# Kernel optimization log

Hardware: AMD Instinct MI355X
Metric: run time of the kernel (lower is better)

## Reference

```python
import jax, jax.numpy as jnp
import numpy as np

B, NH, NPTS = 16, 64, 2048
NEIGHS = 20   # knn neighbors in EdgeConv
K_SEL = 512   # topk points selected
EPS = 1e-5    # BatchNorm eps


def setup_inputs() -> dict:
    key = jax.random.key(0)
    ks = jax.random.split(key, 8)
    xyz = jax.random.normal(ks[0], (B, 3, NPTS), jnp.float32)
    seq1 = jax.random.normal(ks[1], (B, NH, NPTS), jnp.float32)
    perm = jax.random.permutation(ks[2], NPTS)
    # fc: Conv1d(n_h,n_h,1) + BN1d (eval-mode stats)
    W_fc = jax.random.normal(ks[3], (NH, NH), jnp.float32) * 0.1
    b_fc = jnp.zeros((NH,), jnp.float32)
    bn1_gamma = jnp.ones((NH,), jnp.float32)
    bn1_beta = jnp.zeros((NH,), jnp.float32)
    bn1_mean = jnp.zeros((NH,), jnp.float32)
    bn1_var = jnp.ones((NH,), jnp.float32)
    # EdgeConv: Conv2d(2*n_h, n_h, 1, bias=False) + BN2d
    W_ec = jax.random.normal(ks[4], (NH, 2 * NH), jnp.float32) * 0.05
    bn2_gamma = jnp.ones((NH,), jnp.float32)
    bn2_beta = jnp.zeros((NH,), jnp.float32)
    bn2_mean = jnp.zeros((NH,), jnp.float32)
    bn2_var = jnp.ones((NH,), jnp.float32)
    # Discriminator Bilinear(n_h, n_h, 1), xavier-uniform weight, zero bias
    lim = float(np.sqrt(6.0 / (NH + NH)))
    W_b = jax.random.uniform(ks[5], (NH, NH), jnp.float32, -lim, lim)
    b_b = jnp.zeros((), jnp.float32)
    return dict(xyz=xyz, seq1=seq1, perm=perm, W_fc=W_fc, b_fc=b_fc,
                bn1_gamma=bn1_gamma, bn1_beta=bn1_beta, bn1_mean=bn1_mean, bn1_var=bn1_var,
                W_ec=W_ec, bn2_gamma=bn2_gamma, bn2_beta=bn2_beta, bn2_mean=bn2_mean, bn2_var=bn2_var,
                W_b=W_b, b_b=b_b)


def reference(xyz, seq1, perm, W_fc, b_fc, bn1_gamma, bn1_beta, bn1_mean, bn1_var,
              W_ec, bn2_gamma, bn2_beta, bn2_mean, bn2_var, W_b, b_b):
    def fc(x):  # x: [B, NH, N] -> Conv1d(1x1) + BN1d(eval) + ReLU
        y = jnp.einsum('oc,bcn->bon', W_fc, x) + b_fc[None, :, None]
        scale = bn1_gamma / jnp.sqrt(bn1_var + EPS)
        y = (y - bn1_mean[None, :, None]) * scale[None, :, None] + bn1_beta[None, :, None]
        return jax.nn.relu(y)

    seq2 = seq1[:, :, perm]                       # shuffled negative sample
    h1 = fc(seq1)                                 # [B, NH, N]
    h2 = fc(seq2)

    # --- EdgeConv(center): knn in feature space ---
    x2 = jnp.sum(h1 * h1, axis=1)                 # [B, N]
    d = 2.0 * jnp.einsum('bcn,bcm->bnm', h1, h1) - x2[:, :, None] - x2[:, None, :]
    _, nidx = jax.lax.top_k(d, NEIGHS)            # [B, N, K] nearest neighbors

    pts = jnp.transpose(h1, (0, 2, 1))            # [B, N, NH]
    nb = jax.vmap(lambda p, i: p[i])(pts, nidx)   # [B, N, K, NH] gather
    ctr = jnp.broadcast_to(pts[:, :, None, :], nb.shape)
    feat = jnp.concatenate([nb - ctr, ctr], axis=-1)   # [B, N, K, 2*NH]

    y = jnp.einsum('bnkc,oc->bnko', feat, W_ec)   # 1x1 conv
    scale2 = bn2_gamma / jnp.sqrt(bn2_var + EPS)
    y = (y - bn2_mean) * scale2 + bn2_beta        # BN2d over channel (last axis)
    y = jnp.where(y >= 0, y, 0.2 * y)             # LeakyReLU(0.2)
    hn1 = jnp.max(y, axis=2)                      # max over k -> [B, N, NH]

    X = jax.nn.sigmoid(hn1)                       # summary per point, [B, N, NH]

    # --- Discriminator: Bilinear(n_h, n_h, 1) ---
    h1t = pts                                     # [B, N, NH]
    h2t = jnp.transpose(h2, (0, 2, 1))
    sc1 = jnp.einsum('bnc,cd,bnd->bn', h1t, W_b, X) + b_b
    sc2 = jnp.einsum('bnc,cd,bnd->bn', h2t, W_b, X) + b_b
    ret = jnp.concatenate([sc1, sc2], axis=1)     # [B, 2N]

    scores = jax.nn.sigmoid(sc1)                  # ret[:, :N]
    values, idx = jax.lax.top_k(scores, K_SEL)    # [B, K_SEL]

    gi = idx[:, None, :]
    seq_static = jnp.take_along_axis(seq1, jnp.broadcast_to(gi, (B, NH, K_SEL)), axis=2)
    seq = seq_static * values[:, None, :]
    xyz_static = jnp.take_along_axis(xyz, jnp.broadcast_to(gi, (B, 3, K_SEL)), axis=2)
    xyz_out = xyz_static * values[:, None, :]
    return seq, values, idx, ret, xyz_static, xyz_out
```

## Files before the change

kernel.cpp:

```cpp
#include <hip/hip_runtime.h>
#include <math.h>

#define NB 16
#define NH 64
#define NPTS 2048
#define NEIGHS 20
#define KSEL 512
#define EPSV 1e-5f

#define OFF_SEQ 0
#define OFF_VAL (NB*NH*KSEL)
#define OFF_IDX (OFF_VAL + NB*KSEL)
#define OFF_RET (OFF_IDX + NB*KSEL)
#define OFF_XST (OFF_RET + NB*2*NPTS)
#define OFF_XO  (OFF_XST + NB*3*KSEL)

__global__ __launch_bounds__(64) void k_fc(const float* __restrict__ seq1,
                                           const float* __restrict__ Wfc,
                                           const float* __restrict__ bfc,
                                           const float* __restrict__ b1g,
                                           const float* __restrict__ b1b,
                                           const float* __restrict__ b1m,
                                           const float* __restrict__ b1v,
                                           const float* __restrict__ Wec,
                                           float* __restrict__ pts,
                                           float* __restrict__ G1,
                                           float* __restrict__ G2,
                                           float* __restrict__ x2) {
  const int b = blockIdx.y, n0 = blockIdx.x * 64, l = threadIdx.x;
  const int n = n0 + l;
  __shared__ float ptL[64*65];
  const float* sq = seq1 + (size_t)b*NH*NPTS + n;
  float x[64];
  #pragma unroll
  for (int c = 0; c < 64; ++c) x[c] = sq[(size_t)c*NPTS];
  const size_t rowOff = ((size_t)b*NPTS + n)*NH;
  for (int o = 0; o < 64; ++o) {
    float acc = 0.f;
    const float* ar = Wfc + o*64;
    #pragma unroll
    for (int c = 0; c < 64; c += 4) {
      float4 a4 = *(const float4*)(ar + c);
      acc = fmaf(a4.x, x[c],   acc);
      acc = fmaf(a4.y, x[c+1], acc);
      acc = fmaf(a4.z, x[c+2], acc);
      acc = fmaf(a4.w, x[c+3], acc);
    }
    float s1 = b1g[o] / sqrtf(b1v[o] + EPSV);
    float y  = (acc + bfc[o] - b1m[o]) * s1 + b1b[o];
    y = fmaxf(y, 0.f);
    ptL[l*65 + o] = y;
    pts[rowOff + o] = y;
  }
  float pt[64];
  #pragma unroll
  for (int c = 0; c < 64; ++c) pt[c] = ptL[l*65 + c];
  float s2 = 0.f;
  #pragma unroll
  for (int c = 0; c < 64; ++c) s2 = fmaf(pt[c], pt[c], s2);
  x2[(size_t)b*NPTS + n] = s2;
  for (int o = 0; o < 64; ++o) {
    const float* w1 = Wec + o*128;
    float a1 = 0.f, a2 = 0.f;
    #pragma unroll
    for (int c = 0; c < 64; c += 4) {
      float4 u = *(const float4*)(w1 + c);
      float4 v = *(const float4*)(w1 + 64 + c);
      a1 = fmaf(u.x, pt[c],   a1); a1 = fmaf(u.y, pt[c+1], a1);
      a1 = fmaf(u.z, pt[c+2], a1); a1 = fmaf(u.w, pt[c+3], a1);
      a2 = fmaf(v.x, pt[c],   a2); a2 = fmaf(v.y, pt[c+1], a2);
      a2 = fmaf(v.z, pt[c+2], a2); a2 = fmaf(v.w, pt[c+3], a2);
    }
    G1[rowOff + o] = a1;
    G2[rowOff + o] = a2;
  }
}

#define DST 67
#define CSTR 68

__global__ __launch_bounds__(256) void k_knn(const float* __restrict__ pts,
                                             const float* __restrict__ x2,
                                             int* __restrict__ nidx) {
  const int b = blockIdx.y;
  const int row0 = blockIdx.x * 64;
  const int tid = threadIdx.x;
  const int rg = tid >> 4, cg = tid & 15;
  const int l = tid & 63, w = tid >> 6;

  __shared__ float smem[13056];
  float* rowS = smem;
  float* colS = smem + 4352;
  float* dS   = smem + 8704;
  float* x2S  = smem + 12992;

  const float* ptsb = pts + (size_t)b*NPTS*NH;

  {
    int rr = tid & 63, f0 = (tid >> 6) * 16;
    const float* src = ptsb + (size_t)(row0 + rr)*NH + f0;
    #pragma unroll
    for (int q = 0; q < 4; ++q)
      *(float4*)&rowS[rr*CSTR + f0 + 4*q] = *(const float4*)(src + 4*q);
  }

  float Lv[20]; int Li[20];
  #pragma unroll
  for (int k = 0; k < 20; ++k) { Lv[k] = -3.0e38f; Li[k] = 0x7fffffff; }

  for (int ct = 0; ct < NPTS; ct += 64) {
    __syncthreads();
    {
      int cl = tid & 63, f0 = (tid >> 6) * 16;
      const float* src = ptsb + (size_t)(ct + cl)*NH + f0;
      #pragma unroll
      for (int q = 0; q < 4; ++q)
        *(float4*)&colS[cl*CSTR + f0 + 4*q] = *(const float4*)(src + 4*q);
      if (tid < 64) x2S[tid] = x2[(size_t)b*NPTS + ct + tid];
    }
    __syncthreads();
    {
      float acc[4][4];
      #pragma unroll
      for (int i = 0; i < 4; ++i)
        #pragma unroll
        for (int j = 0; j < 4; ++j) acc[i][j] = 0.f;
      #pragma unroll
      for (int c = 0; c < NH; c += 4) {
        float4 rv[4], cv[4];
        #pragma unroll
        for (int i = 0; i < 4; ++i) rv[i] = *(const float4*)&rowS[(rg*4+i)*CSTR + c];
        #pragma unroll
        for (int j = 0; j < 4; ++j) cv[j] = *(const float4*)&colS[(cg+16*j)*CSTR + c];
        #pragma unroll
        for (int i = 0; i < 4; ++i)
          #pragma unroll
          for (int j = 0; j < 4; ++j) {
            acc[i][j] = fmaf(rv[i].x, cv[j].x, acc[i][j]);
            acc[i][j] = fmaf(rv[i].y, cv[j].y, acc[i][j]);
            acc[i][j] = fmaf(rv[i].z, cv[j].z, acc[i][j]);
            acc[i][j] = fmaf(rv[i].w, cv[j].w, acc[i][j]);
          }
      }
      #pragma unroll
      for (int i = 0; i < 4; ++i)
        #pragma unroll
        for (int j = 0; j < 4; ++j) {
          int cc = cg + 16*j;
          dS[(rg*4+i)*DST + cc] = fmaf(2.0f, acc[i][j], -x2S[cc]);
        }
    }
    __syncthreads();
    {
      #pragma unroll
      for (int s = 0; s < 16; ++s) {
        float v = dS[l*DST + w*16 + s];
        int  ci = ct + w*16 + s;
        if (v > Lv[19]) {
          float cv = v; int cidx = ci;
          #pragma unroll
          for (int k = 0; k < 20; ++k) {
            bool c = cv > Lv[k];
            float nv = c ? cv : Lv[k];
            int   ni = c ? cidx : Li[k];
            float ov = Lv[k]; int oi = Li[k];
            cv   = c ? ov : cv;
            cidx = c ? oi : cidx;
            Lv[k] = nv; Li[k] = ni;
          }
        }
      }
    }
  }

  __syncthreads();
  float* mV = smem;
  int*   mI = (int*)smem + 5120;
  #pragma unroll
  for (int k = 0; k < 20; ++k) {
    mV[(w*64 + l)*20 + k] = Lv[k];
    mI[(w*64 + l)*20 + k] = Li[k];
  }
  __syncthreads();
  if (w == 0) {
    for (int ws = 1; ws < 4; ++ws) {
      #pragma unroll
      for (int k = 0; k < 20; ++k) {
        float cv = mV[(ws*64 + l)*20 + k];
        int   ci = mI[(ws*64 + l)*20 + k];
        bool ins = (cv > Lv[19]) || (cv == Lv[19] && ci < Li[19]);
        if (ins) {
          float c0 = cv; int i0 = ci;
          #pragma unroll
          for (int k2 = 0; k2 < 20; ++k2) {
            bool c = (c0 > Lv[k2]) || (c0 == Lv[k2] && i0 < Li[k2]);
            float nv = c ? c0 : Lv[k2];
            int   ni = c ? i0 : Li[k2];
            float ov = Lv[k2]; int oi = Li[k2];
            c0 = c ? ov : c0;
            i0 = c ? oi : i0;
            Lv[k2] = nv; Li[k2] = ni;
          }
        }
      }
    }
    int* dst = nidx + ((size_t)b*NPTS + row0 + l)*NEIGHS;
    #pragma unroll
    for (int k = 0; k < 20; ++k) dst[k] = Li[k];
  }
}

__global__ __launch_bounds__(256) void k_score(const float* __restrict__ pts,
    const float* __restrict__ G1, const float* __restrict__ G2,
    const int* __restrict__ nidx, const int* __restrict__ perm,
    const float* __restrict__ Wb,
    const float* __restrict__ b2g, const float* __restrict__ b2b,
    const float* __restrict__ b2m, const float* __restrict__ b2v,
    const float* __restrict__ bb,
    float* __restrict__ sc1w, float* __restrict__ out) {
  const int b = blockIdx.y;
  const int n0 = blockIdx.x * 16;
  const int tid = threadIdx.x, l = tid & 63, w = tid >> 6;
  __shared__ float WbS[64*65];
  for (int i = tid; i < 64*64; i += 256) WbS[(i >> 6)*65 + (i & 63)] = Wb[i];
  __syncthreads();
  const float sc2v = b2g[l] / sqrtf(b2v[l] + EPSV);
  const float mean2 = b2m[l], beta2 = b2b[l];
  const float bbv = bb[0];
  const float* G1b = G1 + (size_t)b*NPTS*NH;
  for (int it = 0; it < 4; ++it) {
    const int n = n0 + it*4 + w;
    const size_t ro = (size_t)b*NPTS*NH + (size_t)n*NH;
    const float base = G2[ro + l] - G1[ro + l];
    const int* nb = nidx + ((size_t)b*NPTS + n)*NEIGHS;
    float mx = -3.0e38f;
    #pragma unroll
    for (int k = 0; k < NEIGHS; ++k) {
      int m = nb[k];
      float val = G1b[(size_t)m*NH + l] + base;
      float y = (val - mean2) * sc2v + beta2;
      y = (y >= 0.f) ? y : 0.2f*y;
      mx = fmaxf(mx, y);
    }
    float X = 1.f / (1.f + expf(-mx));
    double v = 0.0;
    #pragma unroll
    for (int d = 0; d < 64; ++d) {
      float xd = __shfl(X, d, 64);
      v += (double)WbS[l*65 + d] * (double)xd;
    }
    float p1 = pts[ro + l];
    int pn = perm[n];
    float p2 = pts[(size_t)b*NPTS*NH + (size_t)pn*NH + l];
    double s1 = (double)p1 * v;
    double s2 = (double)p2 * v;
    #pragma unroll
    for (int off = 32; off > 0; off >>= 1) {
      s1 += __shfl_xor(s1, off, 64);
      s2 += __shfl_xor(s2, off, 64);
    }
    if (l == 0) {
      float r1 = (float)(s1 + (double)bbv);
      float r2 = (float)(s2 + (double)bbv);
      sc1w[(size_t)b*NPTS + n] = r1;
      out[OFF_RET + (size_t)b*2*NPTS + n] = r1;
      out[OFF_RET + (size_t)b*2*NPTS + NPTS + n] = r2;
    }
  }
}

__global__ __launch_bounds__(256) void k_select(const float* __restrict__ sc1w,
    const float* __restrict__ seq1, const float* __restrict__ xyz,
    float* __restrict__ out) {
  const int b = blockIdx.x, tid = threadIdx.x;
  __shared__ unsigned long long keys[NPTS];
  __shared__ float valS[KSEL];
  __shared__ int idxS[KSEL];
  for (int i = tid; i < NPTS; i += 256) {
    float f = sc1w[(size_t)b*NPTS + i];
    unsigned u = __float_as_uint(f);
    u = (u & 0x80000000u) ? ~u : (u | 0x80000000u);
    keys[i] = ((unsigned long long)(~u) << 32) | (unsigned)i;
  }
  __syncthreads();
  for (int k = 2; k <= NPTS; k <<= 1) {
    for (int j = k >> 1; j > 0; j >>= 1) {
      for (int i = tid; i < NPTS; i += 256) {
        int l2 = i ^ j;
        if (l2 > i) {
          unsigned long long a = keys[i], c = keys[l2];
          bool up = ((i & k) == 0);
          if ((a > c) == up) { keys[i] = c; keys[l2] = a; }
        }
      }
      __syncthreads();
    }
  }
  for (int i = tid; i < KSEL; i += 256) {
    unsigned long long key = keys[i];
    int sidx = (int)(key & 0xffffffffULL);
    unsigned u = ~(unsigned)(key >> 32);
    unsigned fb = (u & 0x80000000u) ? (u & 0x7fffffffu) : ~u;
    float f = __uint_as_float(fb);
    float val = 1.f / (1.f + expf(-f));
    valS[i] = val; idxS[i] = sidx;
    out[OFF_VAL + (size_t)b*KSEL + i] = val;
    out[OFF_IDX + (size_t)b*KSEL + i] = (float)sidx;
  }
  __syncthreads();
  for (int t = tid; t < NH*KSEL; t += 256) {
    int c = t >> 9, i = t & (KSEL-1);
    float sv = seq1[((size_t)b*NH + c)*NPTS + idxS[i]];
    out[OFF_SEQ + (((size_t)b*NH + c) << 9) + i] = sv * valS[i];
  }
  for (int t = tid; t < 3*KSEL; t += 256) {
    int c = t >> 9, i = t & (KSEL-1);
    float xv = xyz[((size_t)b*3 + c)*NPTS + idxS[i]];
    out[OFF_XST + (((size_t)b*3 + c) << 9) + i] = xv;
    out[OFF_XO  + (((size_t)b*3 + c) << 9) + i] = xv * valS[i];
  }
}

extern "C" void kernel_launch(void* const* d_in, const int* in_sizes, int n_in,
                              void* d_out, int out_size, void* d_ws, size_t ws_size,
                              hipStream_t stream) {
  const float* xyz  = (const float*)d_in[0];
  const float* seq1 = (const float*)d_in[1];
  const int*   perm = (const int*)d_in[2];
  const float* Wfc  = (const float*)d_in[3];
  const float* bfc  = (const float*)d_in[4];
  const float* b1g  = (const float*)d_in[5];
  const float* b1b  = (const float*)d_in[6];
  const float* b1m  = (const float*)d_in[7];
  const float* b1v  = (const float*)d_in[8];
  const float* Wec  = (const float*)d_in[9];
  const float* b2g  = (const float*)d_in[10];
  const float* b2b  = (const float*)d_in[11];
  const float* b2m  = (const float*)d_in[12];
  const float* b2v  = (const float*)d_in[13];
  const float* Wb   = (const float*)d_in[14];
  const float* bb   = (const float*)d_in[15];
  float* out = (float*)d_out;

  float* ws   = (float*)d_ws;
  float* pts  = ws;
  float* G1   = pts + (size_t)NB*NPTS*NH;
  float* G2   = G1  + (size_t)NB*NPTS*NH;
  float* x2   = G2  + (size_t)NB*NPTS*NH;
  float* sc1w = x2  + (size_t)NB*NPTS;
  int*   nidx = (int*)(sc1w + (size_t)NB*NPTS);

  hipLaunchKernelGGL(k_fc, dim3(NPTS/64, NB), dim3(64), 0, stream,
                     seq1, Wfc, bfc, b1g, b1b, b1m, b1v, Wec, pts, G1, G2, x2);
  hipLaunchKernelGGL(k_knn, dim3(NPTS/64, NB), dim3(256), 0, stream,
                     pts, x2, nidx);
  hipLaunchKernelGGL(k_score, dim3(NPTS/16, NB), dim3(256), 0, stream,
                     pts, G1, G2, nidx, perm, Wb, b2g, b2b, b2m, b2v, bb, sc1w, out);
  hipLaunchKernelGGL(k_select, dim3(NB), dim3(256), 0, stream,
                     sc1w, seq1, xyz, out);
}
```

Before: 793.5 us.

## Buffer knn candidates per lane to cut divergent top-20 insertions; coalesce fc stores

In the knn kernel, candidates that beat the current 20th-best go into a small per-lane FIFO of four entries. The full top-20 insertion only runs when some lane in the wave has filled its buffer, so each wave takes the divergent insertion path less often. The fc kernel now stages pts, G1 and G2 through shared memory and writes them transposed so global stores are coalesced, at the cost of extra barriers and a split Wec loop. Buffered candidates are checked against a stale threshold, so more of them may be inserted, and the extra registers could lower occupancy.

```diff
diff --git a/kernel.cpp b/kernel.cpp
--- a/kernel.cpp
+++ b/kernel.cpp
@@ -7,6 +7,7 @@
 #define NEIGHS 20
 #define KSEL 512
 #define EPSV 1e-5f
+#define NINF -3.0e38f
 
 #define OFF_SEQ 0
 #define OFF_VAL (NB*NH*KSEL)
@@ -14,6 +15,23 @@
 #define OFF_RET (OFF_IDX + NB*KSEL)
 #define OFF_XST (OFF_RET + NB*2*NPTS)
 #define OFF_XO  (OFF_XST + NB*3*KSEL)
+
+__device__ __forceinline__ bool better(float av, int ai, float bv, int bi) {
+  return (av > bv) || (av == bv && ai < bi);
+}
+
+__device__ __forceinline__ void ins20(float (&Lv)[20], int (&Li)[20], float cv, int ci) {
+  #pragma unroll
+  for (int k = 0; k < 20; ++k) {
+    bool c = cv > Lv[k];
+    float nv = c ? cv : Lv[k];
+    int   ni = c ? ci : Li[k];
+    float ov = Lv[k]; int oi = Li[k];
+    cv = c ? ov : cv;
+    ci = c ? oi : ci;
+    Lv[k] = nv; Li[k] = ni;
+  }
+}
 
 __global__ __launch_bounds__(64) void k_fc(const float* __restrict__ seq1,
                                            const float* __restrict__ Wfc,
@@ -34,7 +52,7 @@
   float x[64];
   #pragma unroll
   for (int c = 0; c < 64; ++c) x[c] = sq[(size_t)c*NPTS];
-  const size_t rowOff = ((size_t)b*NPTS + n)*NH;
+
   for (int o = 0; o < 64; ++o) {
     float acc = 0.f;
     const float* ar = Wfc + o*64;
@@ -48,32 +66,53 @@
     }
     float s1 = b1g[o] / sqrtf(b1v[o] + EPSV);
     float y  = (acc + bfc[o] - b1m[o]) * s1 + b1b[o];
-    y = fmaxf(y, 0.f);
-    ptL[l*65 + o] = y;
-    pts[rowOff + o] = y;
+    ptL[l*65 + o] = fmaxf(y, 0.f);
   }
   float pt[64];
   #pragma unroll
   for (int c = 0; c < 64; ++c) pt[c] = ptL[l*65 + c];
-  float s2 = 0.f;
-  #pragma unroll
-  for (int c = 0; c < 64; ++c) s2 = fmaf(pt[c], pt[c], s2);
-  x2[(size_t)b*NPTS + n] = s2;
+  {
+    float s2 = 0.f;
+    #pragma unroll
+    for (int c = 0; c < 64; ++c) s2 = fmaf(pt[c], pt[c], s2);
+    x2[(size_t)b*NPTS + n] = s2;
+  }
+  const size_t base = ((size_t)b*NPTS + n0)*NH;
+  __syncthreads();
+  #pragma unroll 4
+  for (int t = 0; t < 64; ++t) pts[base + t*64 + l] = ptL[t*65 + l];
+  __syncthreads();
+
   for (int o = 0; o < 64; ++o) {
     const float* w1 = Wec + o*128;
-    float a1 = 0.f, a2 = 0.f;
+    float a1 = 0.f;
     #pragma unroll
     for (int c = 0; c < 64; c += 4) {
       float4 u = *(const float4*)(w1 + c);
-      float4 v = *(const float4*)(w1 + 64 + c);
       a1 = fmaf(u.x, pt[c],   a1); a1 = fmaf(u.y, pt[c+1], a1);
       a1 = fmaf(u.z, pt[c+2], a1); a1 = fmaf(u.w, pt[c+3], a1);
+    }
+    ptL[l*65 + o] = a1;
+  }
+  __syncthreads();
+  #pragma unroll 4
+  for (int t = 0; t < 64; ++t) G1[base + t*64 + l] = ptL[t*65 + l];
+  __syncthreads();
+
+  for (int o = 0; o < 64; ++o) {
+    const float* w2 = Wec + o*128 + 64;
+    float a2 = 0.f;
+    #pragma unroll
+    for (int c = 0; c < 64; c += 4) {
+      float4 v = *(const float4*)(w2 + c);
       a2 = fmaf(v.x, pt[c],   a2); a2 = fmaf(v.y, pt[c+1], a2);
       a2 = fmaf(v.z, pt[c+2], a2); a2 = fmaf(v.w, pt[c+3], a2);
     }
-    G1[rowOff + o] = a1;
-    G2[rowOff + o] = a2;
-  }
+    ptL[l*65 + o] = a2;
+  }
+  __syncthreads();
+  #pragma unroll 4
+  for (int t = 0; t < 64; ++t) G2[base + t*64 + l] = ptL[t*65 + l];
 }
 
 #define DST 67
@@ -106,16 +145,19 @@
 
   float Lv[20]; int Li[20];
   #pragma unroll
-  for (int k = 0; k < 20; ++k) { Lv[k] = -3.0e38f; Li[k] = 0x7fffffff; }
+  for (int k = 0; k < 20; ++k) { Lv[k] = NINF; Li[k] = 0x7fffffff; }
+  float f0v = NINF, f1v = NINF, f2v = NINF, f3v = NINF;
+  int   f0i = 0,    f1i = 0,    f2i = 0,    f3i = 0;
+  int   cnt = 0;
 
   for (int ct = 0; ct < NPTS; ct += 64) {
     __syncthreads();
     {
-      int cl = tid & 63, f0 = (tid >> 6) * 16;
-      const float* src = ptsb + (size_t)(ct + cl)*NH + f0;
+      int cl = tid & 63, f0_ = (tid >> 6) * 16;
+      const float* src = ptsb + (size_t)(ct + cl)*NH + f0_;
       #pragma unroll
       for (int q = 0; q < 4; ++q)
-        *(float4*)&colS[cl*CSTR + f0 + 4*q] = *(const float4*)(src + 4*q);
+        *(float4*)&colS[cl*CSTR + f0_ + 4*q] = *(const float4*)(src + 4*q);
       if (tid < 64) x2S[tid] = x2[(size_t)b*NPTS + ct + tid];
     }
     __syncthreads();
@@ -152,24 +194,36 @@
     }
     __syncthreads();
     {
+      const float* dRow = dS + l*DST + w*16;
       #pragma unroll
       for (int s = 0; s < 16; ++s) {
-        float v = dS[l*DST + w*16 + s];
+        float v = dRow[s];
         int  ci = ct + w*16 + s;
-        if (v > Lv[19]) {
-          float cv = v; int cidx = ci;
-          #pragma unroll
-          for (int k = 0; k < 20; ++k) {
-            bool c = cv > Lv[k];
-            float nv = c ? cv : Lv[k];
-            int   ni = c ? cidx : Li[k];
-            float ov = Lv[k]; int oi = Li[k];
-            cv   = c ? ov : cv;
-            cidx = c ? oi : cidx;
-            Lv[k] = nv; Li[k] = ni;
+        bool pass = v > Lv[19];
+        f3v = pass ? f2v : f3v;  f3i = pass ? f2i : f3i;
+        f2v = pass ? f1v : f2v;  f2i = pass ? f1i : f2i;
+        f1v = pass ? f0v : f1v;  f1i = pass ? f0i : f1i;
+        f0v = pass ? v   : f0v;  f0i = pass ? ci  : f0i;
+        cnt += pass;
+        if (__any(cnt >= 4)) {
+          #pragma unroll 1
+          for (int e = 3; e >= 0; --e) {
+            float cv = (e==3) ? f3v : (e==2) ? f2v : (e==1) ? f1v : f0v;
+            int  cix = (e==3) ? f3i : (e==2) ? f2i : (e==1) ? f1i : f0i;
+            ins20(Lv, Li, cv, cix);
           }
+          f0v = f1v = f2v = f3v = NINF;
+          cnt = 0;
         }
       }
+    }
+  }
+  {
+    #pragma unroll 1
+    for (int e = 3; e >= 0; --e) {
+      float cv = (e==3) ? f3v : (e==2) ? f2v : (e==1) ? f1v : f0v;
+      int  cix = (e==3) ? f3i : (e==2) ? f2i : (e==1) ? f1i : f0i;
+      ins20(Lv, Li, cv, cix);
     }
   }
 
@@ -188,12 +242,11 @@
       for (int k = 0; k < 20; ++k) {
         float cv = mV[(ws*64 + l)*20 + k];
         int   ci = mI[(ws*64 + l)*20 + k];
-        bool ins = (cv > Lv[19]) || (cv == Lv[19] && ci < Li[19]);
-        if (ins) {
+        if (better(cv, ci, Lv[19], Li[19])) {
           float c0 = cv; int i0 = ci;
           #pragma unroll
           for (int k2 = 0; k2 < 20; ++k2) {
-            bool c = (c0 > Lv[k2]) || (c0 == Lv[k2] && i0 < Li[k2]);
+            bool c = better(c0, i0, Lv[k2], Li[k2]);
             float nv = c ? c0 : Lv[k2];
             int   ni = c ? i0 : Li[k2];
             float ov = Lv[k2]; int oi = Li[k2];
@@ -233,7 +286,7 @@
     const size_t ro = (size_t)b*NPTS*NH + (size_t)n*NH;
     const float base = G2[ro + l] - G1[ro + l];
     const int* nb = nidx + ((size_t)b*NPTS + n)*NEIGHS;
-    float mx = -3.0e38f;
+    float mx = NINF;
     #pragma unroll
     for (int k = 0; k < NEIGHS; ++k) {
       int m = nb[k];
```

Result: faster. 721.6 us (-9.1%).
